# Kernel optimization log

Measured on AMD Instinct MI355X. Metric: run time of the kernel, lower is better.

The kernel has to match this reference:

```python
import jax, jax.numpy as jnp
import numpy as np

MOE_TOP_K = 2
MOE_GATE_NORM_STD = 1.0  # moe_gate_norm_std


def setup_inputs() -> dict:
    key = jax.random.key(0)
    k1, k2, k3, k4 = jax.random.split(key, 4)
    T, D, E = 16384, 2048, 8
    return {
        "x": jax.random.normal(k1, (T, D), dtype=jnp.float32),
        "wg_weight": jax.random.normal(k2, (E, D), dtype=jnp.float32) * 0.02,
        "gate_map_weight": jax.random.normal(k3, (E, E), dtype=jnp.float32) * 0.1,
        "gate_residual": jax.random.normal(k4, (T, E), dtype=jnp.float32),
    }


def reference(x, wg_weight, gate_map_weight, gate_residual):
    # Router GEMM in fp32 (module force-casts wg and input to float32)
    logits = jnp.einsum("td,ed->te", x.astype(jnp.float32), wg_weight)  # [T, E]
    # gate_residual path: gate_map Linear(E, E, bias=False)
    logits = logits + jnp.einsum("te,fe->tf", gate_residual, gate_map_weight)

    num_experts = wg_weight.shape[0]
    # gating(): moe_use_mixtral_gating=False, moe_use_logits_norm=True
    # torch.std is unbiased (ddof=1)
    logits_std = jnp.std(logits, axis=1, keepdims=True, ddof=1)
    probs = jax.nn.softmax(logits / (logits_std / MOE_GATE_NORM_STD), axis=1)
    gates, indices = jax.lax.top_k(probs, MOE_TOP_K)  # [T, K]
    # zero out routing to the last expert, then renormalize
    gates = jnp.where(indices == num_experts - 1, jnp.zeros_like(gates), gates)
    gates = gates / jnp.sum(gates, axis=1, keepdims=True)
    # Dense equivalent of the per-expert nonzero-gather dict: (indices, gates)
    # fully determines expert_info[e] = (tokens where indices==e, matching gates).
    return gates, indices, logits
```

## Files before the change

kernel.cpp:

```cpp
#include <hip/hip_runtime.h>
#include <hip/hip_bf16.h>
#include <stdint.h>


#define DCONST 2048
#define TOK_PER_BATCH 8
#define BATCHES 4

typedef float f32x4 __attribute__((ext_vector_type(4)));

__device__ __forceinline__ unsigned long long shfl_xor_u64(unsigned long long v, int m) {
    int lo = __shfl_xor((int)(uint32_t)v, m, 64);
    int hi = __shfl_xor((int)(uint32_t)(v >> 32), m, 64);
    return ((unsigned long long)(uint32_t)hi << 32) | (unsigned long long)(uint32_t)lo;
}

__global__ __launch_bounds__(256, 2)
void router_gemm(const float* __restrict__ x,
                 const float* __restrict__ wg,
                 float* __restrict__ ws,
                 int T)
{
    const int wave  = threadIdx.x >> 6;
    const int lane  = threadIdx.x & 63;
    const int W     = blockIdx.x * 4 + wave;
    const int g     = W & 7;
    const int tbase = (W >> 3) * 32;

    const float* wgp = wg + g * 256 + (lane << 2);
    f32x4 w8[8];
    #pragma unroll
    for (int e = 0; e < 8; ++e)
        w8[e] = *(const f32x4*)(wgp + (size_t)e * DCONST);

    const float* xp = x + (size_t)tbase * DCONST + g * 256 + (lane << 2);

    f32x4 xa[4], xb[4];

    #define LOADH(buf, trow)                                                  \
        { _Pragma("unroll")                                                   \
          for (int i = 0; i < 4; ++i)                                         \
              buf[i] = __builtin_nontemporal_load(                            \
                  (const f32x4*)(xp + (size_t)((trow) + i) * DCONST)); }

    #define FMAH(buf, tloc0)                                                  \
        { _Pragma("unroll")                                                   \
          for (int i = 0; i < 4; ++i) {                                       \
              _Pragma("unroll")                                               \
              for (int e = 0; e < 8; ++e) {                                   \
                  float a = acc[((tloc0) + i) * 8 + e];                       \
                  a += buf[i].x * w8[e].x;                                    \
                  a += buf[i].y * w8[e].y;                                    \
                  a += buf[i].z * w8[e].z;                                    \
                  a += buf[i].w * w8[e].w;                                    \
                  acc[((tloc0) + i) * 8 + e] = a;                             \
              }                                                               \
          } }

    LOADH(xa, 0);
    LOADH(xb, 4);

    #pragma unroll 1
    for (int b = 0; b < BATCHES; ++b) {
        float acc[64];
        #pragma unroll
        for (int v = 0; v < 64; ++v) acc[v] = 0.f;

        FMAH(xa, 0);
        if (b < BATCHES - 1) LOADH(xa, (b + 1) * 8);
        FMAH(xb, 4);
        if (b < BATCHES - 1) LOADH(xb, (b + 1) * 8 + 4);

        #pragma unroll
        for (int m = 1; m < 64; m <<= 1) {
            const bool up = (lane & m) != 0;
            #pragma unroll
            for (int v = 0; v < 64; v += 2 * m) {
                const float keep = up ? acc[v + m] : acc[v];
                const float send = up ? acc[v] : acc[v + m];
                const float got  = __shfl_xor(send, m, 64);
                acc[v] = keep + got;
            }
        }

        const int tb = (tbase + b * TOK_PER_BATCH) >> 3;
        ws[(size_t)tb * 512 + g * 64 + lane] = acc[0];
    }
}

__global__ __launch_bounds__(256)
void router_epilogue(const float* __restrict__ ws,
                     const float* __restrict__ gm,
                     const float* __restrict__ gr,
                     float* __restrict__ out,
                     int T)
{
    const int wave = threadIdx.x >> 6;
    const int lane = threadIdx.x & 63;
    const int tb   = blockIdx.x * 4 + wave;
    const int t0   = tb * 8;

    float logit = 0.f;
    #pragma unroll
    for (int g = 0; g < 8; ++g)
        logit += ws[(size_t)tb * 512 + g * 64 + lane];

    const int tt = lane >> 3;
    const int f  = lane & 7;
    const int t  = t0 + tt;

    const float4 ga = *(const float4*)(gr + (size_t)t * 8);
    const float4 gb = *(const float4*)(gr + (size_t)t * 8 + 4);
    const float4 ma = *(const float4*)(gm + f * 8);
    const float4 mb = *(const float4*)(gm + f * 8 + 4);
    logit += ga.x * ma.x + ga.y * ma.y + ga.z * ma.z + ga.w * ma.w
           + gb.x * mb.x + gb.y * mb.y + gb.z * mb.z + gb.w * mb.w;

    out[(size_t)4 * T + (size_t)t0 * 8 + lane] = logit;

    float s = logit;
    s += __shfl_xor(s, 1, 64);
    s += __shfl_xor(s, 2, 64);
    s += __shfl_xor(s, 4, 64);
    const float mean = s * 0.125f;
    float d2 = (logit - mean) * (logit - mean);
    d2 += __shfl_xor(d2, 1, 64);
    d2 += __shfl_xor(d2, 2, 64);
    d2 += __shfl_xor(d2, 4, 64);
    const float stdv = sqrtf(d2 / 7.0f);

    uint32_t ob = __float_as_uint(logit);
    ob = (ob & 0x80000000u) ? ~ob : (ob | 0x80000000u);
    unsigned long long k1 = ((unsigned long long)ob << 8) | (unsigned long long)(7 - f);
    unsigned long long k2 = 0ull;
    #pragma unroll
    for (int m = 1; m <= 4; m <<= 1) {
        const unsigned long long o1 = shfl_xor_u64(k1, m);
        const unsigned long long o2 = shfl_xor_u64(k2, m);
        const unsigned long long hi = k1 > o1 ? k1 : o1;
        const unsigned long long lo = k1 > o1 ? o1 : k1;
        const unsigned long long so = k2 > o2 ? k2 : o2;
        k1 = hi;
        k2 = lo > so ? lo : so;
    }
    const int i1 = 7 - (int)(k1 & 0xFFull);
    const int i2 = 7 - (int)(k2 & 0xFFull);
    uint32_t b1 = (uint32_t)(k1 >> 8), b2 = (uint32_t)(k2 >> 8);
    b1 = (b1 & 0x80000000u) ? (b1 ^ 0x80000000u) : ~b1;
    b2 = (b2 & 0x80000000u) ? (b2 ^ 0x80000000u) : ~b2;
    const float l1 = __uint_as_float(b1);
    const float l2 = __uint_as_float(b2);

    float g0, g1;
    if (i1 == 7)      { g0 = 0.f; g1 = 1.f; }
    else if (i2 == 7) { g0 = 1.f; g1 = 0.f; }
    else {
        const float p = 1.0f / (1.0f + __expf(-(l1 - l2) / stdv));
        g0 = p; g1 = 1.0f - p;
    }

    if (f == 0) out[(size_t)2 * t]             = g0;
    if (f == 1) out[(size_t)2 * t + 1]         = g1;
    if (f == 2) out[(size_t)2 * T + 2 * t]     = (float)i1;
    if (f == 3) out[(size_t)2 * T + 2 * t + 1] = (float)i2;
}

extern "C" void kernel_launch(void* const* d_in, const int* in_sizes, int n_in,
                              void* d_out, int out_size, void* d_ws, size_t ws_size,
                              hipStream_t stream) {
    const float* x  = (const float*)d_in[0];
    const float* wg = (const float*)d_in[1];
    const float* gm = (const float*)d_in[2];
    const float* gr = (const float*)d_in[3];
    float* ws = (float*)d_ws;
    const int T = in_sizes[0] / DCONST;

    const int gemm_blocks = (8 * (T / 32)) / 4;
    router_gemm<<<gemm_blocks, 256, 0, stream>>>(x, wg, ws, T);

    const int epi_blocks = T / 32;
    router_epilogue<<<epi_blocks, 256, 0, stream>>>(ws, gm, gr, (float*)d_out, T);
}
```

Baseline: 190.3 us.

## Fuse router GEMM and epilogue into one kernel via shared-memory reduction

Merges the two kernels into a single launch. Each 512-thread block handles 32 tokens, with one wave per D-slice, and the partial sums are reduced through LDS instead of a global workspace. This removes a kernel launch and the workspace write and read round trip. In exchange, half the threads sit idle during the epilogue, and the __syncthreads plus the larger block may reduce occupancy.

```diff
diff --git a/kernel.cpp b/kernel.cpp
--- a/kernel.cpp
+++ b/kernel.cpp
@@ -1,5 +1,4 @@
 #include <hip/hip_runtime.h>
-#include <hip/hip_bf16.h>
 #include <stdint.h>
 
 
@@ -15,17 +14,20 @@
     return ((unsigned long long)(uint32_t)hi << 32) | (unsigned long long)(uint32_t)lo;
 }
 
-__global__ __launch_bounds__(256, 2)
-void router_gemm(const float* __restrict__ x,
-                 const float* __restrict__ wg,
-                 float* __restrict__ ws,
-                 int T)
+__global__ __launch_bounds__(512, 2)
+void router_fused(const float* __restrict__ x,
+                  const float* __restrict__ wg,
+                  const float* __restrict__ gm,
+                  const float* __restrict__ gr,
+                  float* __restrict__ out,
+                  int T)
 {
     const int wave  = threadIdx.x >> 6;
     const int lane  = threadIdx.x & 63;
-    const int W     = blockIdx.x * 4 + wave;
-    const int g     = W & 7;
-    const int tbase = (W >> 3) * 32;
+    const int g     = wave;
+    const int tbase = blockIdx.x * 32;
+
+    __shared__ float red[8 * 256];
 
     const float* wgp = wg + g * 256 + (lane << 2);
     f32x4 w8[8];
@@ -83,86 +85,77 @@
             }
         }
 
-        const int tb = (tbase + b * TOK_PER_BATCH) >> 3;
-        ws[(size_t)tb * 512 + g * 64 + lane] = acc[0];
-    }
-}
-
-__global__ __launch_bounds__(256)
-void router_epilogue(const float* __restrict__ ws,
-                     const float* __restrict__ gm,
-                     const float* __restrict__ gr,
-                     float* __restrict__ out,
-                     int T)
-{
-    const int wave = threadIdx.x >> 6;
-    const int lane = threadIdx.x & 63;
-    const int tb   = blockIdx.x * 4 + wave;
-    const int t0   = tb * 8;
-
-    float logit = 0.f;
-    #pragma unroll
-    for (int g = 0; g < 8; ++g)
-        logit += ws[(size_t)tb * 512 + g * 64 + lane];
-
-    const int tt = lane >> 3;
-    const int f  = lane & 7;
-    const int t  = t0 + tt;
-
-    const float4 ga = *(const float4*)(gr + (size_t)t * 8);
-    const float4 gb = *(const float4*)(gr + (size_t)t * 8 + 4);
-    const float4 ma = *(const float4*)(gm + f * 8);
-    const float4 mb = *(const float4*)(gm + f * 8 + 4);
-    logit += ga.x * ma.x + ga.y * ma.y + ga.z * ma.z + ga.w * ma.w
-           + gb.x * mb.x + gb.y * mb.y + gb.z * mb.z + gb.w * mb.w;
-
-    out[(size_t)4 * T + (size_t)t0 * 8 + lane] = logit;
-
-    float s = logit;
-    s += __shfl_xor(s, 1, 64);
-    s += __shfl_xor(s, 2, 64);
-    s += __shfl_xor(s, 4, 64);
-    const float mean = s * 0.125f;
-    float d2 = (logit - mean) * (logit - mean);
-    d2 += __shfl_xor(d2, 1, 64);
-    d2 += __shfl_xor(d2, 2, 64);
-    d2 += __shfl_xor(d2, 4, 64);
-    const float stdv = sqrtf(d2 / 7.0f);
-
-    uint32_t ob = __float_as_uint(logit);
-    ob = (ob & 0x80000000u) ? ~ob : (ob | 0x80000000u);
-    unsigned long long k1 = ((unsigned long long)ob << 8) | (unsigned long long)(7 - f);
-    unsigned long long k2 = 0ull;
-    #pragma unroll
-    for (int m = 1; m <= 4; m <<= 1) {
-        const unsigned long long o1 = shfl_xor_u64(k1, m);
-        const unsigned long long o2 = shfl_xor_u64(k2, m);
-        const unsigned long long hi = k1 > o1 ? k1 : o1;
-        const unsigned long long lo = k1 > o1 ? o1 : k1;
-        const unsigned long long so = k2 > o2 ? k2 : o2;
-        k1 = hi;
-        k2 = lo > so ? lo : so;
-    }
-    const int i1 = 7 - (int)(k1 & 0xFFull);
-    const int i2 = 7 - (int)(k2 & 0xFFull);
-    uint32_t b1 = (uint32_t)(k1 >> 8), b2 = (uint32_t)(k2 >> 8);
-    b1 = (b1 & 0x80000000u) ? (b1 ^ 0x80000000u) : ~b1;
-    b2 = (b2 & 0x80000000u) ? (b2 ^ 0x80000000u) : ~b2;
-    const float l1 = __uint_as_float(b1);
-    const float l2 = __uint_as_float(b2);
-
-    float g0, g1;
-    if (i1 == 7)      { g0 = 0.f; g1 = 1.f; }
-    else if (i2 == 7) { g0 = 1.f; g1 = 0.f; }
-    else {
-        const float p = 1.0f / (1.0f + __expf(-(l1 - l2) / stdv));
-        g0 = p; g1 = 1.0f - p;
+        red[wave * 256 + b * 64 + lane] = acc[0];
     }
 
-    if (f == 0) out[(size_t)2 * t]             = g0;
-    if (f == 1) out[(size_t)2 * t + 1]         = g1;
-    if (f == 2) out[(size_t)2 * T + 2 * t]     = (float)i1;
-    if (f == 3) out[(size_t)2 * T + 2 * t + 1] = (float)i2;
+    __syncthreads();
+
+    const int tid = threadIdx.x;
+    if (tid < 256) {
+        const int f  = lane & 7;
+        const int tt = lane >> 3;
+        const int t  = tbase + wave * 8 + tt;
+
+        float logit = 0.f;
+        #pragma unroll
+        for (int w = 0; w < 8; ++w)
+            logit += red[w * 256 + tid];
+
+        const float4 ga = *(const float4*)(gr + (size_t)t * 8);
+        const float4 gb = *(const float4*)(gr + (size_t)t * 8 + 4);
+        const float4 ma = *(const float4*)(gm + f * 8);
+        const float4 mb = *(const float4*)(gm + f * 8 + 4);
+        logit += ga.x * ma.x + ga.y * ma.y + ga.z * ma.z + ga.w * ma.w
+               + gb.x * mb.x + gb.y * mb.y + gb.z * mb.z + gb.w * mb.w;
+
+        out[(size_t)4 * T + (size_t)tbase * 8 + tid] = logit;
+
+        float s = logit;
+        s += __shfl_xor(s, 1, 64);
+        s += __shfl_xor(s, 2, 64);
+        s += __shfl_xor(s, 4, 64);
+        const float mean = s * 0.125f;
+        float d2 = (logit - mean) * (logit - mean);
+        d2 += __shfl_xor(d2, 1, 64);
+        d2 += __shfl_xor(d2, 2, 64);
+        d2 += __shfl_xor(d2, 4, 64);
+        const float stdv = sqrtf(d2 / 7.0f);
+
+        uint32_t ob = __float_as_uint(logit);
+        ob = (ob & 0x80000000u) ? ~ob : (ob | 0x80000000u);
+        unsigned long long k1 = ((unsigned long long)ob << 8) | (unsigned long long)(7 - f);
+        unsigned long long k2 = 0ull;
+        #pragma unroll
+        for (int m = 1; m <= 4; m <<= 1) {
+            const unsigned long long o1 = shfl_xor_u64(k1, m);
+            const unsigned long long o2 = shfl_xor_u64(k2, m);
+            const unsigned long long hi = k1 > o1 ? k1 : o1;
+            const unsigned long long lo = k1 > o1 ? o1 : k1;
+            const unsigned long long so = k2 > o2 ? k2 : o2;
+            k1 = hi;
+            k2 = lo > so ? lo : so;
+        }
+        const int i1 = 7 - (int)(k1 & 0xFFull);
+        const int i2 = 7 - (int)(k2 & 0xFFull);
+        uint32_t b1 = (uint32_t)(k1 >> 8), b2 = (uint32_t)(k2 >> 8);
+        b1 = (b1 & 0x80000000u) ? (b1 ^ 0x80000000u) : ~b1;
+        b2 = (b2 & 0x80000000u) ? (b2 ^ 0x80000000u) : ~b2;
+        const float l1 = __uint_as_float(b1);
+        const float l2 = __uint_as_float(b2);
+
+        float g0, g1;
+        if (i1 == 7)      { g0 = 0.f; g1 = 1.f; }
+        else if (i2 == 7) { g0 = 1.f; g1 = 0.f; }
+        else {
+            const float p = 1.0f / (1.0f + __expf(-(l1 - l2) / stdv));
+            g0 = p; g1 = 1.0f - p;
+        }
+
+        if (f == 0) out[(size_t)2 * t]             = g0;
+        if (f == 1) out[(size_t)2 * t + 1]         = g1;
+        if (f == 2) out[(size_t)2 * T + 2 * t]     = (float)i1;
+        if (f == 3) out[(size_t)2 * T + 2 * t + 1] = (float)i2;
+    }
 }
 
 extern "C" void kernel_launch(void* const* d_in, const int* in_sizes, int n_in,
@@ -172,12 +165,9 @@
     const float* wg = (const float*)d_in[1];
     const float* gm = (const float*)d_in[2];
     const float* gr = (const float*)d_in[3];
-    float* ws = (float*)d_ws;
     const int T = in_sizes[0] / DCONST;
 
-    const int gemm_blocks = (8 * (T / 32)) / 4;
-    router_gemm<<<gemm_blocks, 256, 0, stream>>>(x, wg, ws, T);
-
-    const int epi_blocks = T / 32;
-    router_epilogue<<<epi_blocks, 256, 0, stream>>>(ws, gm, gr, (float*)d_out, T);
+    const int blocks = T / 32;
+    router_fused<<<blocks, 512, 0, stream>>>(x, wg, gm, gr, (float*)out_size ? (float*)d_out : (float*)d_out, T);
+    (void)d_ws; (void)ws_size; (void)n_in;
 }
```

Measured after the change: 195.3 us. 2.6% more time.

## Split router GEMM reduction into two 32-accumulator halves to double occupancy

Applied to the files above, without the earlier changes.

Each batch of 8 tokens is now processed as two halves of 4 tokens, each with a 32-entry accumulator reduced by a 5-step butterfly plus one cross-half shuffle. Launch bounds go from 2 to 4 blocks per SIMD. The aim is to cut register pressure so more waves are resident to hide the streaming loads of x. The trade is extra shuffles and serialized reductions per batch, and lanes now pick the result from the matching half.

```diff
diff --git a/kernel.cpp b/kernel.cpp
--- a/kernel.cpp
+++ b/kernel.cpp
@@ -1,5 +1,4 @@
 #include <hip/hip_runtime.h>
-#include <hip/hip_bf16.h>
 #include <stdint.h>
 
 
@@ -15,7 +14,7 @@
     return ((unsigned long long)(uint32_t)hi << 32) | (unsigned long long)(uint32_t)lo;
 }
 
-__global__ __launch_bounds__(256, 2)
+__global__ __launch_bounds__(256, 4)
 void router_gemm(const float* __restrict__ x,
                  const float* __restrict__ wg,
                  float* __restrict__ ws,
@@ -43,48 +42,56 @@
               buf[i] = __builtin_nontemporal_load(                            \
                   (const f32x4*)(xp + (size_t)((trow) + i) * DCONST)); }
 
-    #define FMAH(buf, tloc0)                                                  \
+    #define FMAH4(buf)                                                        \
         { _Pragma("unroll")                                                   \
           for (int i = 0; i < 4; ++i) {                                       \
               _Pragma("unroll")                                               \
               for (int e = 0; e < 8; ++e) {                                   \
-                  float a = acc[((tloc0) + i) * 8 + e];                       \
+                  float a = acc[i * 8 + e];                                   \
                   a += buf[i].x * w8[e].x;                                    \
                   a += buf[i].y * w8[e].y;                                    \
                   a += buf[i].z * w8[e].z;                                    \
                   a += buf[i].w * w8[e].w;                                    \
-                  acc[((tloc0) + i) * 8 + e] = a;                             \
+                  acc[i * 8 + e] = a;                                         \
               }                                                               \
           } }
+
+    #define BFLY32(result)                                                    \
+        { _Pragma("unroll")                                                   \
+          for (int m = 1; m < 32; m <<= 1) {                                  \
+              const bool up = (lane & m) != 0;                                \
+              _Pragma("unroll")                                               \
+              for (int v = 0; v < 32; v += 2 * m) {                           \
+                  const float keep = up ? acc[v + m] : acc[v];                \
+                  const float send = up ? acc[v] : acc[v + m];                \
+                  const float got  = __shfl_xor(send, m, 64);                 \
+                  acc[v] = keep + got;                                        \
+              }                                                               \
+          }                                                                   \
+          result = acc[0] + __shfl_xor(acc[0], 32, 64); }
 
     LOADH(xa, 0);
     LOADH(xb, 4);
 
     #pragma unroll 1
     for (int b = 0; b < BATCHES; ++b) {
-        float acc[64];
-        #pragma unroll
-        for (int v = 0; v < 64; ++v) acc[v] = 0.f;
-
-        FMAH(xa, 0);
-        if (b < BATCHES - 1) LOADH(xa, (b + 1) * 8);
-        FMAH(xb, 4);
-        if (b < BATCHES - 1) LOADH(xb, (b + 1) * 8 + 4);
+        float acc[32];
+        float hA, hB;
 
         #pragma unroll
-        for (int m = 1; m < 64; m <<= 1) {
-            const bool up = (lane & m) != 0;
-            #pragma unroll
-            for (int v = 0; v < 64; v += 2 * m) {
-                const float keep = up ? acc[v + m] : acc[v];
-                const float send = up ? acc[v] : acc[v + m];
-                const float got  = __shfl_xor(send, m, 64);
-                acc[v] = keep + got;
-            }
-        }
+        for (int v = 0; v < 32; ++v) acc[v] = 0.f;
+        FMAH4(xa);
+        if (b < BATCHES - 1) LOADH(xa, (b + 1) * 8);
+        BFLY32(hA);
+
+        #pragma unroll
+        for (int v = 0; v < 32; ++v) acc[v] = 0.f;
+        FMAH4(xb);
+        if (b < BATCHES - 1) LOADH(xb, (b + 1) * 8 + 4);
+        BFLY32(hB);
 
         const int tb = (tbase + b * TOK_PER_BATCH) >> 3;
-        ws[(size_t)tb * 512 + g * 64 + lane] = acc[0];
+        ws[(size_t)tb * 512 + g * 64 + lane] = (lane < 32) ? hA : hB;
     }
 }
 
```

New measurement: 637.5 us. +234.9%, slower.
